# Kernel optimization log

Hardware: AMD Instinct MI355X
Metric: run time of the kernel (lower is better)

## Reference

```python
import jax, jax.numpy as jnp
import numpy as np

B, S, D = 4, 4096, 1024


def setup_inputs() -> dict:
    key = jax.random.key(0)
    kx, kq, kk, kv = jax.random.split(key, 4)
    x = jax.random.normal(kx, (B, S, D), dtype=jnp.float32)
    W_q = jax.random.normal(kq, (D, D), dtype=jnp.float32) / np.sqrt(D)
    W_k = jax.random.normal(kk, (D, D), dtype=jnp.float32) / np.sqrt(D)
    W_v = jax.random.normal(kv, (D, D), dtype=jnp.float32) / np.sqrt(D)
    return {"x": x, "W_q": W_q, "W_k": W_k, "W_v": W_v}


def reference(x, W_q, W_k, W_v):
    # Projections: [B,S,D] @ [D,D] -> [B,S,D]
    Q = jnp.einsum('bsd,de->bse', x, W_q)
    K = jnp.einsum('bsd,de->bse', x, W_k)
    V = jnp.einsum('bsd,de->bse', x, W_v)
    scale = 1.0 / np.sqrt(D).astype(np.float32)
    # scores [B,S,S]; flash-attention computes softmax(QK^T/sqrt(d)) V exactly,
    # with rowmax/rowsum maintained in tiles -- mathematically identical to this.
    scores = jnp.einsum('bqd,bkd->bqk', Q, K) * scale
    probs = jax.nn.softmax(scores, axis=-1)
    out = jnp.einsum('bqk,bkd->bqd', probs, V)  # [B,S,D]
    return out
```

## Files before the change

kernel.cpp:

```cpp
#include <hip/hip_runtime.h>
#include <hip/hip_bf16.h>
#include <hip/hip_fp16.h>
#include <stdint.h>
#include <stddef.h>

typedef __attribute__((ext_vector_type(4))) float f32x4;
typedef __attribute__((ext_vector_type(8))) short s16x8;
typedef __attribute__((ext_vector_type(4))) short s16x4;

#define AS1 __attribute__((address_space(1)))
#define AS3 __attribute__((address_space(3)))

static __device__ __forceinline__ void gload_lds16(const void* g, void* l) {
  __builtin_amdgcn_global_load_lds((const AS1 void*)g, (AS3 void*)l, 16, 0, 0);
}

static __device__ __forceinline__ short bf16_bits(float f) {
  __hip_bfloat16 h = __float2bfloat16(f);
  union { __hip_bfloat16 h; short s; } u; u.h = h; return u.s;
}
static __device__ __forceinline__ short f16_bits(float f) {
  __half h = __float2half(f);
  union { __half h; short s; } u; u.h = h; return u.s;
}
static __device__ __forceinline__ float f16_to_f32(short b) {
  union { short s; __half h; } u; u.s = b; return __half2float(u.h);
}

#define WAITVM8   asm volatile("s_waitcnt vmcnt(8)" ::: "memory")
#define WAITVM4   asm volatile("s_waitcnt vmcnt(4)" ::: "memory")
#define WAITVM0   asm volatile("s_waitcnt vmcnt(0)" ::: "memory")
#define WAITLGKM0 asm volatile("s_waitcnt lgkmcnt(0)" ::: "memory")
#define SCHEDB    __builtin_amdgcn_sched_barrier(0)
#define SBAR      __builtin_amdgcn_s_barrier()

template<int EPI>
__global__ __launch_bounds__(512, 2) void gemm256_bt(
    const __hip_bfloat16* __restrict__ A,
    const __hip_bfloat16* __restrict__ Bt,
    void* __restrict__ Cv,
    int M, int N, int Kd,
    long zsA, long zsB, long zsC)
{
  __shared__ __hip_bfloat16 lds[3][2][256][32];
  A  += (long)blockIdx.z * zsA;
  Bt += (long)blockIdx.z * zsB;

  const int tid  = threadIdx.x;
  const int lane = tid & 63;
  const int wid  = tid >> 6;
  const int wm   = wid >> 2;
  const int wn   = wid & 3;
  const long bm  = (long)blockIdx.y * 256;
  const long bn  = (long)blockIdx.x * 256;

  const int lrow  = lane >> 2;
  const int pslot = lane & 3;

  f32x4 acc[8][4];
#pragma unroll
  for (int i = 0; i < 8; ++i)
#pragma unroll
    for (int j = 0; j < 4; ++j)
      acc[i][j] = (f32x4){0.f, 0.f, 0.f, 0.f};

  const int NK = Kd >> 5;

#define STAGE256(b, kt)                                                        \
  {                                                                            \
    _Pragma("unroll")                                                          \
    for (int half = 0; half < 2; ++half) {                                     \
      const int r  = wid * 32 + half * 16 + lrow;                              \
      const int ks = (pslot - ((r >> 1) & 3)) & 3;                             \
      const int kA = ((kt) << 5) + (ks << 3);                                  \
      gload_lds16(A  + (size_t)(bm + r) * Kd + kA,                             \
                  &lds[b][0][wid * 32 + half * 16][0]);                        \
      gload_lds16(Bt + (size_t)(bn + r) * Kd + kA,                             \
                  &lds[b][1][wid * 32 + half * 16][0]);                        \
    }                                                                          \
  }

  STAGE256(0, 0);
  if (NK > 1) STAGE256(1, 1);

  int buf = 0;
  int sb  = 2;

  const int frow  = lane & 15;
  const int fslot = lane >> 4;

  for (int i = 0; i < NK; ++i) {
    if (i + 2 < NK) {
      STAGE256(sb, i + 2);
      WAITVM8;
    } else if (i + 2 == NK) {
      WAITVM4;
    } else {
      WAITVM0;
    }
    SCHEDB;
    SBAR;
    SCHEDB;

    s16x8 bfv[4];
#pragma unroll
    for (int ni = 0; ni < 4; ++ni) {
      const int r = wn * 64 + ni * 16 + frow;
      bfv[ni] = *(const s16x8*)&lds[buf][1][r][((fslot + (r >> 1)) & 3) << 3];
    }
    __builtin_amdgcn_s_setprio(1);
#pragma unroll
    for (int mi = 0; mi < 8; ++mi) {
      const int r = wm * 128 + mi * 16 + frow;
      const s16x8 af =
          *(const s16x8*)&lds[buf][0][r][((fslot + (r >> 1)) & 3) << 3];
#pragma unroll
      for (int ni = 0; ni < 4; ++ni)
        acc[mi][ni] = __builtin_amdgcn_mfma_f32_16x16x32_bf16(
            af, bfv[ni], acc[mi][ni], 0, 0, 0);
    }
    __builtin_amdgcn_s_setprio(0);

    WAITLGKM0;
    SCHEDB;
    SBAR;
    SCHEDB;

    buf = (buf == 2) ? 0 : buf + 1;
    sb  = (sb  == 2) ? 0 : sb  + 1;
  }

  const int col   = lane & 15;
  const int rquad = (lane >> 4) << 2;
#pragma unroll
  for (int mi = 0; mi < 8; ++mi) {
#pragma unroll
    for (int ni = 0; ni < 4; ++ni) {
      const long m0 = bm + wm * 128 + mi * 16 + rquad;
      const long n  = bn + wn * 64 + ni * 16 + col;
#pragma unroll
      for (int j = 0; j < 4; ++j) {
        const float v = acc[mi][ni][j];
        if (EPI == 1) {
          float* C = (float*)Cv + (long)blockIdx.z * zsC;
          C[(size_t)(m0 + j) * N + n] = v;
        } else if (EPI == 4) {
          short* C = (short*)Cv + (long)blockIdx.z * zsC;
          C[(size_t)(m0 + j) * N + n] = f16_bits(v);
        } else {
          const int route = (int)(bn >> 10);
          __hip_bfloat16* base = (__hip_bfloat16*)Cv + (long)route * 16777216L;
          const long nl = n & 1023;
          const long m  = m0 + j;
          if (route < 2) {
            base[(size_t)m * 1024 + nl] = __float2bfloat16(v);
          } else {
            const long b = m >> 12;
            const long s = m & 4095;
            base[(((b << 10) + nl) << 12) + s] = __float2bfloat16(v);
          }
        }
      }
    }
  }
}

__global__ __launch_bounds__(256) void cvt_f32_bf16(
    const float* __restrict__ x, __hip_bfloat16* __restrict__ o, long n)
{
  const long i = ((long)blockIdx.x * 256 + threadIdx.x) * 8;
  if (i >= n) return;
  f32x4 a = *(const f32x4*)(x + i);
  f32x4 b = *(const f32x4*)(x + i + 4);
  s16x8 r;
  r[0] = bf16_bits(a.x); r[1] = bf16_bits(a.y);
  r[2] = bf16_bits(a.z); r[3] = bf16_bits(a.w);
  r[4] = bf16_bits(b.x); r[5] = bf16_bits(b.y);
  r[6] = bf16_bits(b.z); r[7] = bf16_bits(b.w);
  *(s16x8*)((short*)o + i) = r;
}

__global__ __launch_bounds__(256) void transpose_w_bf16(
    const float* __restrict__ W, __hip_bfloat16* __restrict__ Wt)
{
  __shared__ float t[32][33];
  const int tx = threadIdx.x & 31;
  const int ty = (threadIdx.x >> 5) * 4;
  const int bx = blockIdx.x * 32;
  const int by = blockIdx.y * 32;
#pragma unroll
  for (int j = 0; j < 4; ++j)
    t[ty + j][tx] = W[(size_t)(by + ty + j) * 1024 + bx + tx];
  __syncthreads();
#pragma unroll
  for (int j = 0; j < 4; ++j)
    Wt[(size_t)(bx + ty + j) * 1024 + by + tx] = __float2bfloat16(t[tx][ty + j]);
}

__global__ __launch_bounds__(256) void softmax_inplace(
    short* __restrict__ scP, float scale)
{
  __shared__ float red[4];
  const int t = threadIdx.x;
  short* pr = scP + (long)blockIdx.x * 4096;

  s16x8 h0 = *(const s16x8*)(pr + t * 8);
  s16x8 h1 = *(const s16x8*)(pr + 2048 + t * 8);
  float v[16];
  float mx = -3.4e38f;
#pragma unroll
  for (int j = 0; j < 8; ++j) { v[j]     = f16_to_f32(h0[j]); }
#pragma unroll
  for (int j = 0; j < 8; ++j) { v[8 + j] = f16_to_f32(h1[j]); }
#pragma unroll
  for (int i = 0; i < 16; ++i) mx = fmaxf(mx, v[i]);
#pragma unroll
  for (int off = 32; off >= 1; off >>= 1) mx = fmaxf(mx, __shfl_xor(mx, off));
  if ((t & 63) == 0) red[t >> 6] = mx;
  __syncthreads();
  mx = fmaxf(fmaxf(red[0], red[1]), fmaxf(red[2], red[3]));
  __syncthreads();

  float sum = 0.f;
#pragma unroll
  for (int i = 0; i < 16; ++i) { v[i] = __expf((v[i] - mx) * scale); sum += v[i]; }
#pragma unroll
  for (int off = 32; off >= 1; off >>= 1) sum += __shfl_xor(sum, off);
  if ((t & 63) == 0) red[t >> 6] = sum;
  __syncthreads();
  sum = red[0] + red[1] + red[2] + red[3];
  const float inv = 1.f / sum;

  s16x8 o0, o1;
#pragma unroll
  for (int j = 0; j < 8; ++j) { o0[j] = bf16_bits(v[j] * inv); }
#pragma unroll
  for (int j = 0; j < 8; ++j) { o1[j] = bf16_bits(v[8 + j] * inv); }
  *(s16x8*)(pr + t * 8) = o0;
  *(s16x8*)(pr + 2048 + t * 8) = o1;
}

extern "C" void kernel_launch(void* const* d_in, const int* in_sizes, int n_in,
                              void* d_out, int out_size, void* d_ws, size_t ws_size,
                              hipStream_t stream) {
  (void)in_sizes; (void)n_in; (void)out_size; (void)ws_size;
  const float* x  = (const float*)d_in[0];
  const float* Wq = (const float*)d_in[1];
  const float* Wk = (const float*)d_in[2];
  const float* Wv = (const float*)d_in[3];
  float* out = (float*)d_out;

  char* ws = (char*)d_ws;
  __hip_bfloat16* qb  = (__hip_bfloat16*)(ws);
  __hip_bfloat16* kb  = (__hip_bfloat16*)(ws + 33554432L);
  __hip_bfloat16* vt  = (__hip_bfloat16*)(ws + 67108864L);
  __hip_bfloat16* wt  = (__hip_bfloat16*)(ws + 100663296L);
  short*          scP = (short*)         (ws + 106954752L);
  __hip_bfloat16* xb  = (__hip_bfloat16*)(ws + 106954752L);

  cvt_f32_bf16<<<8192, 256, 0, stream>>>(x, xb, 16777216L);
  transpose_w_bf16<<<dim3(32, 32), 256, 0, stream>>>(Wq, wt);
  transpose_w_bf16<<<dim3(32, 32), 256, 0, stream>>>(Wk, wt + 1048576L);
  transpose_w_bf16<<<dim3(32, 32), 256, 0, stream>>>(Wv, wt + 2097152L);

  gemm256_bt<3><<<dim3(12, 64, 1), 512, 0, stream>>>(
      xb, wt, qb, 16384, 3072, 1024, 0L, 0L, 0L);

  gemm256_bt<4><<<dim3(16, 16, 4), 512, 0, stream>>>(
      qb, kb, scP, 4096, 4096, 1024,
      4194304L, 4194304L, 16777216L);

  softmax_inplace<<<16384, 256, 0, stream>>>(scP, 0.03125f);

  gemm256_bt<1><<<dim3(4, 16, 4), 512, 0, stream>>>(
      (const __hip_bfloat16*)scP, vt, out, 4096, 1024, 4096,
      16777216L, 4194304L, 4194304L);
}
```

Baseline: 629.0 us.

## Swizzle block-to-tile mapping for XCD locality and split MFMA loop with barrier

Adds a template parameter that remaps the linear block index so blocks landing on the same XCD (lin & 7) cover nearby tiles, for the QK^T and PV GEMMs. The goal is better L2 reuse of shared A/B tiles across the chiplets. It also splits the inner MFMA loop into two halves with an extra s_barrier between them, to keep waves in lockstep and stagger LDS reads. The extra barrier adds sync overhead, and the remap relies on the exact grid shapes.

```diff
diff --git a/kernel.cpp b/kernel.cpp
--- a/kernel.cpp
+++ b/kernel.cpp
@@ -34,7 +34,7 @@
 #define SCHEDB    __builtin_amdgcn_sched_barrier(0)
 #define SBAR      __builtin_amdgcn_s_barrier()
 
-template<int EPI>
+template<int EPI, int SWZ>
 __global__ __launch_bounds__(512, 2) void gemm256_bt(
     const __hip_bfloat16* __restrict__ A,
     const __hip_bfloat16* __restrict__ Bt,
@@ -43,16 +43,37 @@
     long zsA, long zsB, long zsC)
 {
   __shared__ __hip_bfloat16 lds[3][2][256][32];
-  A  += (long)blockIdx.z * zsA;
-  Bt += (long)blockIdx.z * zsB;
+
+  int bx, by, bz;
+  if (SWZ == 1) {
+    const int lin = blockIdx.x + (blockIdx.y << 4) + (blockIdx.z << 8);
+    const int x7  = lin & 7;
+    const int idx = (lin >> 3) & 31;
+    bz = lin >> 8;
+    by = ((x7 & 3) << 2) + (idx & 3);
+    bx = ((x7 >> 2) << 3) + (idx >> 2);
+  } else if (SWZ == 2) {
+    const int lin = blockIdx.x + (blockIdx.y << 2) + (blockIdx.z << 6);
+    const int x7  = lin & 7;
+    const int idx = (lin >> 3) & 31;
+    const int zb  = (x7 << 1) + (idx >> 4);
+    bz = zb >> 2;
+    bx = zb & 3;
+    by = idx & 15;
+  } else {
+    bx = blockIdx.x; by = blockIdx.y; bz = blockIdx.z;
+  }
+
+  A  += (long)bz * zsA;
+  Bt += (long)bz * zsB;
 
   const int tid  = threadIdx.x;
   const int lane = tid & 63;
   const int wid  = tid >> 6;
   const int wm   = wid >> 2;
   const int wn   = wid & 3;
-  const long bm  = (long)blockIdx.y * 256;
-  const long bn  = (long)blockIdx.x * 256;
+  const long bm  = (long)by * 256;
+  const long bn  = (long)bx * 256;
 
   const int lrow  = lane >> 2;
   const int pslot = lane & 3;
@@ -110,7 +131,22 @@
     }
     __builtin_amdgcn_s_setprio(1);
 #pragma unroll
-    for (int mi = 0; mi < 8; ++mi) {
+    for (int mi = 0; mi < 4; ++mi) {
+      const int r = wm * 128 + mi * 16 + frow;
+      const s16x8 af =
+          *(const s16x8*)&lds[buf][0][r][((fslot + (r >> 1)) & 3) << 3];
+#pragma unroll
+      for (int ni = 0; ni < 4; ++ni)
+        acc[mi][ni] = __builtin_amdgcn_mfma_f32_16x16x32_bf16(
+            af, bfv[ni], acc[mi][ni], 0, 0, 0);
+    }
+    __builtin_amdgcn_s_setprio(0);
+
+    SBAR;
+
+    __builtin_amdgcn_s_setprio(1);
+#pragma unroll
+    for (int mi = 4; mi < 8; ++mi) {
       const int r = wm * 128 + mi * 16 + frow;
       const s16x8 af =
           *(const s16x8*)&lds[buf][0][r][((fslot + (r >> 1)) & 3) << 3];
@@ -142,10 +178,10 @@
       for (int j = 0; j < 4; ++j) {
         const float v = acc[mi][ni][j];
         if (EPI == 1) {
-          float* C = (float*)Cv + (long)blockIdx.z * zsC;
+          float* C = (float*)Cv + (long)bz * zsC;
           C[(size_t)(m0 + j) * N + n] = v;
         } else if (EPI == 4) {
-          short* C = (short*)Cv + (long)blockIdx.z * zsC;
+          short* C = (short*)Cv + (long)bz * zsC;
           C[(size_t)(m0 + j) * N + n] = f16_bits(v);
         } else {
           const int route = (int)(bn >> 10);
@@ -263,16 +299,16 @@
   transpose_w_bf16<<<dim3(32, 32), 256, 0, stream>>>(Wk, wt + 1048576L);
   transpose_w_bf16<<<dim3(32, 32), 256, 0, stream>>>(Wv, wt + 2097152L);
 
-  gemm256_bt<3><<<dim3(12, 64, 1), 512, 0, stream>>>(
+  gemm256_bt<3, 0><<<dim3(12, 64, 1), 512, 0, stream>>>(
       xb, wt, qb, 16384, 3072, 1024, 0L, 0L, 0L);
 
-  gemm256_bt<4><<<dim3(16, 16, 4), 512, 0, stream>>>(
+  gemm256_bt<4, 1><<<dim3(16, 16, 4), 512, 0, stream>>>(
       qb, kb, scP, 4096, 4096, 1024,
       4194304L, 4194304L, 16777216L);
 
   softmax_inplace<<<16384, 256, 0, stream>>>(scP, 0.03125f);
 
-  gemm256_bt<1><<<dim3(4, 16, 4), 512, 0, stream>>>(
+  gemm256_bt<1, 2><<<dim3(4, 16, 4), 512, 0, stream>>>(
       (const __hip_bfloat16*)scP, vt, out, 4096, 1024, 4096,
       16777216L, 4194304L, 4194304L);
 }
```

Result: faster. 593.0 us (-5.7%).
